# Performance work log

Hardware: AMD Instinct MI355X
Metric: run time of the kernel (lower is better)

Reference implementation:

```python
import jax, jax.numpy as jnp
import numpy as np

B, S, D, H = 2, 2048, 512, 8
DK = D // H


def setup_inputs() -> dict:
    key = jax.random.key(0)
    ks = jax.random.split(key, 7)
    scale = 1.0 / np.sqrt(D)
    return {
        "query": jax.random.normal(ks[0], (B, S, D), dtype=jnp.float32),
        "key": jax.random.normal(ks[1], (B, S, D), dtype=jnp.float32),
        "value": jax.random.normal(ks[2], (B, S, D), dtype=jnp.float32),
        "w_q": jax.random.normal(ks[3], (D, D), dtype=jnp.float32) * scale,
        "w_k": jax.random.normal(ks[4], (D, D), dtype=jnp.float32) * scale,
        "w_v": jax.random.normal(ks[5], (D, D), dtype=jnp.float32) * scale,
        "w_o": jax.random.normal(ks[6], (D, D), dtype=jnp.float32) * scale,
    }


def reference(query, key, value, w_q, w_k, w_v, w_o):
    # Linear projections (torch nn.Linear: x @ W.T), split into heads -> [b, h, s, dk]
    def proj(x, w):
        return (x @ w.T).reshape(B, -1, H, DK).transpose(0, 2, 1, 3)

    q = proj(query, w_q)
    k = proj(key, w_k)
    v = proj(value, w_v)

    # scaled dot-product attention (unfused, materializes [b,h,s,s] scores)
    scores = jnp.einsum("bhqd,bhkd->bhqk", q, k) / np.sqrt(DK)
    p_attn = jax.nn.softmax(scores, axis=-1)
    out = jnp.einsum("bhqk,bhkd->bhqd", p_attn, v)  # [b,h,s,dk]

    # merge heads and final projection
    out = out.transpose(0, 2, 1, 3).reshape(B, -1, D)
    out = out @ w_o.T
    return (out, p_attn)
```

## Files before the change

### kernel.cpp

```cpp
#include <hip/hip_runtime.h>
#include <hip/hip_bf16.h>
#include <cstdint>
#include <cstddef>

#define BB 2
#define SS 2048
#define DD 512
#define HH 8
#define DKK 64

typedef __attribute__((ext_vector_type(8))) short bf16x8;
typedef __attribute__((ext_vector_type(4))) float f32x4;

__device__ __forceinline__ unsigned short f2bf(float f) {
    union { float f; unsigned u; } v; v.f = f;
    unsigned u = v.u;
    return (unsigned short)((u + 0x7fffu + ((u >> 16) & 1u)) >> 16);
}
__device__ __forceinline__ unsigned pack2(float a, float b) {
    return (unsigned)f2bf(a) | ((unsigned)f2bf(b) << 16);
}

typedef const __attribute__((address_space(1))) unsigned int* gp_t;
typedef __attribute__((address_space(3))) unsigned int* lp_t;
__device__ __forceinline__ void gload_lds16(const void* g, void* l) {
    __builtin_amdgcn_global_load_lds((gp_t)g, (lp_t)l, 16, 0, 0);
}

#define VM_WAIT4 asm volatile("s_waitcnt vmcnt(4)" ::: "memory")
#define VM_WAIT0 asm volatile("s_waitcnt vmcnt(0)" ::: "memory")

__global__ __launch_bounds__(256) void k_cvt(
    const float* __restrict__ q, const float* __restrict__ k, const float* __restrict__ v,
    const float* __restrict__ wq, const float* __restrict__ wk, const float* __restrict__ wv,
    const float* __restrict__ wo, unsigned short* __restrict__ dst,
    unsigned short* __restrict__ dwo)
{
    const size_t NX = (size_t)BB * SS * DD;
    const size_t NW = (size_t)DD * DD;
    const int y = blockIdx.y;
    const float* src; unsigned short* d; int n;
    switch (y) {
        case 0: src = q;  d = dst;                 n = (int)NX; break;
        case 1: src = k;  d = dst + NX;            n = (int)NX; break;
        case 2: src = v;  d = dst + 2 * NX;        n = (int)NX; break;
        case 3: src = wq; d = dst + 3 * NX;        n = (int)NW; break;
        case 4: src = wk; d = dst + 3 * NX + NW;   n = (int)NW; break;
        case 5: src = wv; d = dst + 3 * NX + 2*NW; n = (int)NW; break;
        default: src = wo; d = dwo;                n = (int)NW; break;
    }
    int idx = (blockIdx.x * 256 + threadIdx.x) * 8;
    if (idx >= n) return;
    float4 a = *(const float4*)(src + idx);
    float4 b = *(const float4*)(src + idx + 4);
    *(uint4*)(d + idx) = make_uint4(pack2(a.x,a.y), pack2(a.z,a.w), pack2(b.x,b.y), pack2(b.z,b.w));
}

__device__ __forceinline__ void gemm64_core(
    const unsigned short* __restrict__ A, const unsigned short* __restrict__ W,
    unsigned short* smem, int bm, int bn, int tid, f32x4 acc[4])
{
    const int w = tid >> 6, lane = tid & 63, quad = lane >> 4, l15 = lane & 15;
    for (int k0 = 0; k0 < DD; k0 += 64) {
        #pragma unroll
        for (int r = 0; r < 2; ++r) {
            int flat = r * 256 + tid;
            int row = flat >> 3, c = flat & 7, cs = c ^ (row & 7);
            gload_lds16(A + (size_t)(bm * 64 + row) * DD + k0 + cs * 8, &smem[flat * 8]);
        }
        #pragma unroll
        for (int r = 0; r < 2; ++r) {
            int flat = r * 256 + tid;
            int row = flat >> 3, c = flat & 7, cs = c ^ (row & 7);
            gload_lds16(W + (size_t)(bn * 64 + row) * DD + k0 + cs * 8, &smem[4096 + flat * 8]);
        }
        __syncthreads();
        int mrow = w * 16 + l15;
        bf16x8 a0 = *(const bf16x8*)&smem[(mrow * 8 + (quad ^ (mrow & 7))) * 8];
        bf16x8 a1 = *(const bf16x8*)&smem[(mrow * 8 + ((quad + 4) ^ (mrow & 7))) * 8];
        #pragma unroll
        for (int nt = 0; nt < 4; ++nt) {
            int nrow = nt * 16 + l15;
            bf16x8 b0 = *(const bf16x8*)&smem[4096 + (nrow * 8 + (quad ^ (nrow & 7))) * 8];
            bf16x8 b1 = *(const bf16x8*)&smem[4096 + (nrow * 8 + ((quad + 4) ^ (nrow & 7))) * 8];
            acc[nt] = __builtin_amdgcn_mfma_f32_16x16x32_bf16(a0, b0, acc[nt], 0, 0, 0);
            acc[nt] = __builtin_amdgcn_mfma_f32_16x16x32_bf16(a1, b1, acc[nt], 0, 0, 0);
        }
        __syncthreads();
    }
}

__global__ __launch_bounds__(256) void k_gemm_qkv(
    const unsigned short* __restrict__ scratch,
    unsigned short* __restrict__ Qw, unsigned short* __restrict__ Kw,
    unsigned short* __restrict__ Vt)
{
    __shared__ unsigned short smem[8192];
    const size_t NX = (size_t)BB * SS * DD, NW = (size_t)DD * DD;
    const int z = blockIdx.z;
    const unsigned short* A = scratch + (size_t)z * NX;
    const unsigned short* W = scratch + 3 * NX + (size_t)z * NW;
    const int bm = blockIdx.x, bn = blockIdx.y;
    const int tid = threadIdx.x, w = tid >> 6, lane = tid & 63, quad = lane >> 4, l15 = lane & 15;

    f32x4 acc[4];
    #pragma unroll
    for (int i = 0; i < 4; ++i) acc[i] = (f32x4){0.f, 0.f, 0.f, 0.f};
    gemm64_core(A, W, smem, bm, bn, tid, acc);

    if (z != 2) {
        const float sc = (z == 0) ? 0.125f : 1.0f;
        unsigned short* dbf = (z == 0) ? Qw : Kw;
        #pragma unroll
        for (int nt = 0; nt < 4; ++nt) {
            int n = bn * 64 + nt * 16 + l15;
            int h = n >> 6, dk = n & 63;
            #pragma unroll
            for (int rg = 0; rg < 4; ++rg) {
                int m = bm * 64 + w * 16 + quad * 4 + rg;
                int b = m >> 11, s = m & (SS - 1);
                dbf[(((size_t)(b * HH + h) * SS + s) << 6) + dk] = f2bf(acc[nt][rg] * sc);
            }
        }
    } else {
        unsigned short* T = smem;
        #pragma unroll
        for (int nt = 0; nt < 4; ++nt)
            #pragma unroll
            for (int rg = 0; rg < 4; ++rg)
                T[(w * 16 + quad * 4 + rg) * 72 + nt * 16 + l15] = f2bf(acc[nt][rg]);
        __syncthreads();
        int n = tid >> 2, s0 = (tid & 3) * 16;
        int ng = bn * 64 + n, h = ng >> 6, dk = ng & 63;
        int mg = bm * 64 + s0, b = mg >> 11, s = mg & (SS - 1);
        unsigned vals[8];
        #pragma unroll
        for (int i = 0; i < 8; ++i)
            vals[i] = (unsigned)T[(s0 + 2*i) * 72 + n] | ((unsigned)T[(s0 + 2*i + 1) * 72 + n] << 16);
        unsigned short* dp = Vt + ((size_t)(b * HH + h) * DKK + dk) * SS + s;
        ((uint4*)dp)[0] = make_uint4(vals[0], vals[1], vals[2], vals[3]);
        ((uint4*)dp)[1] = make_uint4(vals[4], vals[5], vals[6], vals[7]);
    }
}

__global__ __launch_bounds__(256) void k_attn(
    const unsigned short* __restrict__ Qw, const unsigned short* __restrict__ Kw,
    const unsigned short* __restrict__ Vt, unsigned short* __restrict__ AO,
    float* __restrict__ Linv)
{
    __shared__ unsigned short Kl[2][4096];
    __shared__ unsigned short Vl[2][4096];
    __shared__ unsigned short Pl[2][4][16][68];

    const int id = blockIdx.x;
    const int xcd = id & 7, j = id >> 3;
    const int bh = xcd * 2 + (j >> 5), qt = j & 31;

    const int tid = threadIdx.x, w = tid >> 6, lane = tid & 63, quad = lane >> 4, l15 = lane & 15;

    const unsigned short* Qb = Qw + ((size_t)bh * SS + qt * 64 + w * 16) * DKK;
    const unsigned short* Kb = Kw + (size_t)bh * SS * DKK;
    const unsigned short* Vb = Vt + (size_t)bh * DKK * SS;

    bf16x8 qa0 = *(const bf16x8*)&Qb[l15 * DKK + quad * 8];
    bf16x8 qa1 = *(const bf16x8*)&Qb[l15 * DKK + 32 + quad * 8];

    f32x4 oacc[4];
    #pragma unroll
    for (int i = 0; i < 4; ++i) oacc[i] = (f32x4){0.f, 0.f, 0.f, 0.f};
    float lsum[4] = {0.f, 0.f, 0.f, 0.f};

    auto stage = [&](int kt, int b) {
        #pragma unroll
        for (int r = 0; r < 2; ++r) {
            int flat = r * 256 + tid;
            int row = flat >> 3, c = flat & 7, cs = c ^ (row & 7);
            gload_lds16(Kb + (size_t)(kt * 64 + row) * DKK + cs * 8, &Kl[b][flat * 8]);
        }
        #pragma unroll
        for (int r = 0; r < 2; ++r) {
            int flat = r * 256 + tid;
            int row = flat >> 3, c = flat & 7, cs = c ^ (row & 7);
            gload_lds16(Vb + (size_t)row * SS + kt * 64 + cs * 8, &Vl[b][flat * 8]);
        }
    };

    stage(0, 0);
    stage(1, 1);

    const int NT = SS / 64;
    for (int kt = 0; kt < NT; ++kt) {
        if (kt < NT - 1) { VM_WAIT4; } else { VM_WAIT0; }
        __builtin_amdgcn_s_barrier();
        __builtin_amdgcn_sched_barrier(0);
        const int b = kt & 1;

        f32x4 sa[4];
        #pragma unroll
        for (int i = 0; i < 4; ++i) sa[i] = (f32x4){0.f, 0.f, 0.f, 0.f};
        __builtin_amdgcn_s_setprio(1);
        #pragma unroll
        for (int jt = 0; jt < 4; ++jt) {
            int row = jt * 16 + l15;
            bf16x8 b0 = *(const bf16x8*)&Kl[b][(row * 8 + (quad ^ (row & 7))) * 8];
            bf16x8 b1 = *(const bf16x8*)&Kl[b][(row * 8 + ((quad + 4) ^ (row & 7))) * 8];
            sa[jt] = __builtin_amdgcn_mfma_f32_16x16x32_bf16(qa0, b0, sa[jt], 0, 0, 0);
            sa[jt] = __builtin_amdgcn_mfma_f32_16x16x32_bf16(qa1, b1, sa[jt], 0, 0, 0);
        }
        __builtin_amdgcn_s_setprio(0);

        float ev[4][4];
        #pragma unroll
        for (int jt = 0; jt < 4; ++jt)
            #pragma unroll
            for (int rg = 0; rg < 4; ++rg)
                ev[jt][rg] = __expf(sa[jt][rg]);
        #pragma unroll
        for (int rg = 0; rg < 4; ++rg) {
            float s = ev[0][rg] + ev[1][rg] + ev[2][rg] + ev[3][rg];
            s += __shfl_xor(s, 1);
            s += __shfl_xor(s, 2);
            s += __shfl_xor(s, 4);
            s += __shfl_xor(s, 8);
            lsum[rg] += s;
        }
        #pragma unroll
        for (int jt = 0; jt < 4; ++jt)
            #pragma unroll
            for (int rg = 0; rg < 4; ++rg)
                Pl[b][w][quad * 4 + rg][jt * 16 + l15] = f2bf(ev[jt][rg]);
        bf16x8 pa0 = *(const bf16x8*)&Pl[b][w][l15][quad * 8];
        bf16x8 pa1 = *(const bf16x8*)&Pl[b][w][l15][32 + quad * 8];

        __builtin_amdgcn_s_setprio(1);
        #pragma unroll
        for (int dt = 0; dt < 4; ++dt) {
            int row = dt * 16 + l15;
            bf16x8 v0 = *(const bf16x8*)&Vl[b][(row * 8 + (quad ^ (row & 7))) * 8];
            bf16x8 v1 = *(const bf16x8*)&Vl[b][(row * 8 + ((quad + 4) ^ (row & 7))) * 8];
            oacc[dt] = __builtin_amdgcn_mfma_f32_16x16x32_bf16(pa0, v0, oacc[dt], 0, 0, 0);
            oacc[dt] = __builtin_amdgcn_mfma_f32_16x16x32_bf16(pa1, v1, oacc[dt], 0, 0, 0);
        }
        __builtin_amdgcn_s_setprio(0);

        __builtin_amdgcn_s_barrier();
        if (kt + 2 < NT) stage(kt + 2, b);
    }

    float linv[4];
    #pragma unroll
    for (int rg = 0; rg < 4; ++rg) linv[rg] = 1.0f / lsum[rg];

    const int b2 = bh >> 3, h = bh & 7;
    const int srow = qt * 64 + w * 16 + quad * 4;
    #pragma unroll
    for (int dt = 0; dt < 4; ++dt)
        #pragma unroll
        for (int rg = 0; rg < 4; ++rg)
            AO[((size_t)(b2 * SS + srow + rg) << 9) + h * 64 + dt * 16 + l15] =
                f2bf(oacc[dt][rg] * linv[rg]);

    if (l15 == 0) {
        #pragma unroll
        for (int rg = 0; rg < 4; ++rg)
            Linv[(size_t)bh * SS + srow + rg] = linv[rg];
    }
}

__global__ __launch_bounds__(256) void k_pwrite(
    const unsigned short* __restrict__ Qw, const unsigned short* __restrict__ Kw,
    const float* __restrict__ Linv, float* __restrict__ P)
{
    __shared__ float Tl[4][16][68];
    const int id = blockIdx.x;
    const int xcd = id & 7, j = id >> 3;
    const int bh = xcd * 2 + (j >> 7);
    const int rem = j & 127, qt = rem >> 2, ks = rem & 3;
    const int tid = threadIdx.x, w = tid >> 6, lane = tid & 63, quad = lane >> 4, l15 = lane & 15;

    const unsigned short* Qb = Qw + ((size_t)bh * SS + qt * 64 + w * 16) * DKK;
    bf16x8 qa0 = *(const bf16x8*)&Qb[l15 * DKK + quad * 8];
    bf16x8 qa1 = *(const bf16x8*)&Qb[l15 * DKK + 32 + quad * 8];

    float linv[4];
    #pragma unroll
    for (int rg = 0; rg < 4; ++rg)
        linv[rg] = Linv[(size_t)bh * SS + qt * 64 + w * 16 + quad * 4 + rg];

    const unsigned short* Kb = Kw + (size_t)bh * SS * DKK + (size_t)ks * 512 * DKK;
    float* Pb = P + (((size_t)bh * SS + qt * 64 + w * 16) << 11) + ks * 512;

    for (int kt = 0; kt < 8; ++kt) {
        const unsigned short* Kt = Kb + (size_t)kt * 64 * DKK;
        #pragma unroll
        for (int jt = 0; jt < 4; ++jt) {
            bf16x8 b0 = *(const bf16x8*)&Kt[(jt * 16 + l15) * DKK + quad * 8];
            bf16x8 b1 = *(const bf16x8*)&Kt[(jt * 16 + l15) * DKK + 32 + quad * 8];
            f32x4 sa = (f32x4){0.f, 0.f, 0.f, 0.f};
            sa = __builtin_amdgcn_mfma_f32_16x16x32_bf16(qa0, b0, sa, 0, 0, 0);
            sa = __builtin_amdgcn_mfma_f32_16x16x32_bf16(qa1, b1, sa, 0, 0, 0);
            #pragma unroll
            for (int rg = 0; rg < 4; ++rg)
                Tl[w][quad * 4 + rg][jt * 16 + l15] = __expf(sa[rg]) * linv[rg];
        }
        #pragma unroll
        for (int c = 0; c < 4; ++c) {
            int row = c * 4 + quad;
            f32x4 val = *(const f32x4*)&Tl[w][row][l15 * 4];
            __builtin_nontemporal_store(val,
                (f32x4*)(Pb + ((size_t)row << 11) + kt * 64 + l15 * 4));
        }
    }
}

__global__ __launch_bounds__(256) void k_gemm_o(
    const unsigned short* __restrict__ A, const unsigned short* __restrict__ W,
    float* __restrict__ out)
{
    __shared__ unsigned short smem[8192];
    const int bm = blockIdx.x, bn = blockIdx.y;
    const int tid = threadIdx.x, w = tid >> 6, lane = tid & 63, quad = lane >> 4, l15 = lane & 15;
    f32x4 acc[4];
    #pragma unroll
    for (int i = 0; i < 4; ++i) acc[i] = (f32x4){0.f, 0.f, 0.f, 0.f};
    gemm64_core(A, W, smem, bm, bn, tid, acc);
    #pragma unroll
    for (int nt = 0; nt < 4; ++nt)
        #pragma unroll
        for (int rg = 0; rg < 4; ++rg)
            out[(size_t)(bm * 64 + w * 16 + quad * 4 + rg) * DD + bn * 64 + nt * 16 + l15] =
                acc[nt][rg];
}

extern "C" void kernel_launch(void* const* d_in, const int* in_sizes, int n_in,
                              void* d_out, int out_size, void* d_ws, size_t ws_size,
                              hipStream_t stream) {
    const float* q  = (const float*)d_in[0];
    const float* k  = (const float*)d_in[1];
    const float* v  = (const float*)d_in[2];
    const float* wq = (const float*)d_in[3];
    const float* wk = (const float*)d_in[4];
    const float* wv = (const float*)d_in[5];
    const float* wo = (const float*)d_in[6];

    float* out = (float*)d_out;
    float* P   = out + (size_t)BB * SS * DD;

    const size_t NX = (size_t)BB * SS * DD;
    const size_t NW = (size_t)DD * DD;

    unsigned short* scratch = (unsigned short*)P;

    unsigned short* Qw   = (unsigned short*)d_ws;
    unsigned short* Kw   = Qw + NX;
    unsigned short* Vt   = Kw + NX;
    unsigned short* AO   = Vt + NX;
    unsigned short* Wo2  = AO + NX;
    float*          Linv = (float*)(Wo2 + NW);

    k_cvt<<<dim3(1024, 7), 256, 0, stream>>>(q, k, v, wq, wk, wv, wo, scratch, Wo2);
    k_gemm_qkv<<<dim3(64, 8, 3), 256, 0, stream>>>(scratch, Qw, Kw, Vt);
    k_attn<<<dim3(512), 256, 0, stream>>>(Qw, Kw, Vt, AO, Linv);
    k_pwrite<<<dim3(2048), 256, 0, stream>>>(Qw, Kw, Linv, P);
    k_gemm_o<<<dim3(64, 8), 256, 0, stream>>>(AO, Wo2, out);
}
```

Before: 393.5 us.

## Fuse fp32-to-bf16 conversion into GEMM tile loads with register prefetch

Removes the separate conversion kernel. The QKV and output projection GEMMs now read fp32 inputs and weights directly, convert them to bf16 in registers, and write them into LDS. The next k-tile is loaded into registers while the current one is computed, giving a simple software pipeline. This drops one launch and the write and re-read of a bf16 scratch copy. In exchange, weights are re-read and re-converted by every block in fp32, so global traffic per tile doubles, and register pressure goes up.

```diff
diff --git a/kernel.cpp b/kernel.cpp
--- a/kernel.cpp
+++ b/kernel.cpp
@@ -30,51 +30,63 @@
 #define VM_WAIT4 asm volatile("s_waitcnt vmcnt(4)" ::: "memory")
 #define VM_WAIT0 asm volatile("s_waitcnt vmcnt(0)" ::: "memory")
 
-__global__ __launch_bounds__(256) void k_cvt(
-    const float* __restrict__ q, const float* __restrict__ k, const float* __restrict__ v,
-    const float* __restrict__ wq, const float* __restrict__ wk, const float* __restrict__ wv,
-    const float* __restrict__ wo, unsigned short* __restrict__ dst,
-    unsigned short* __restrict__ dwo)
-{
-    const size_t NX = (size_t)BB * SS * DD;
-    const size_t NW = (size_t)DD * DD;
-    const int y = blockIdx.y;
-    const float* src; unsigned short* d; int n;
-    switch (y) {
-        case 0: src = q;  d = dst;                 n = (int)NX; break;
-        case 1: src = k;  d = dst + NX;            n = (int)NX; break;
-        case 2: src = v;  d = dst + 2 * NX;        n = (int)NX; break;
-        case 3: src = wq; d = dst + 3 * NX;        n = (int)NW; break;
-        case 4: src = wk; d = dst + 3 * NX + NW;   n = (int)NW; break;
-        case 5: src = wv; d = dst + 3 * NX + 2*NW; n = (int)NW; break;
-        default: src = wo; d = dwo;                n = (int)NW; break;
-    }
-    int idx = (blockIdx.x * 256 + threadIdx.x) * 8;
-    if (idx >= n) return;
-    float4 a = *(const float4*)(src + idx);
-    float4 b = *(const float4*)(src + idx + 4);
-    *(uint4*)(d + idx) = make_uint4(pack2(a.x,a.y), pack2(a.z,a.w), pack2(b.x,b.y), pack2(b.z,b.w));
-}
-
-__device__ __forceinline__ void gemm64_core(
-    const unsigned short* __restrict__ A, const unsigned short* __restrict__ W,
+template <bool ABF>
+__device__ __forceinline__ void gemm64_core2(
+    const void* __restrict__ Av, const float* __restrict__ W,
     unsigned short* smem, int bm, int bn, int tid, f32x4 acc[4])
 {
     const int w = tid >> 6, lane = tid & 63, quad = lane >> 4, l15 = lane & 15;
-    for (int k0 = 0; k0 < DD; k0 += 64) {
+
+    float4 ra[2][2], rw[2][2];
+    auto loadRegs = [&](int k0) {
+        if (!ABF) {
+            const float* A = (const float*)Av;
+            #pragma unroll
+            for (int r = 0; r < 2; ++r) {
+                int flat = r * 256 + tid;
+                int row = flat >> 3, c = flat & 7, cs = c ^ (row & 7);
+                const float* p = A + (size_t)(bm * 64 + row) * DD + k0 + cs * 8;
+                ra[r][0] = *(const float4*)p;
+                ra[r][1] = *(const float4*)(p + 4);
+            }
+        }
         #pragma unroll
         for (int r = 0; r < 2; ++r) {
             int flat = r * 256 + tid;
             int row = flat >> 3, c = flat & 7, cs = c ^ (row & 7);
-            gload_lds16(A + (size_t)(bm * 64 + row) * DD + k0 + cs * 8, &smem[flat * 8]);
-        }
+            const float* p = W + (size_t)(bn * 64 + row) * DD + k0 + cs * 8;
+            rw[r][0] = *(const float4*)p;
+            rw[r][1] = *(const float4*)(p + 4);
+        }
+    };
+    auto writeLDS = [&]() {
         #pragma unroll
         for (int r = 0; r < 2; ++r) {
             int flat = r * 256 + tid;
-            int row = flat >> 3, c = flat & 7, cs = c ^ (row & 7);
-            gload_lds16(W + (size_t)(bn * 64 + row) * DD + k0 + cs * 8, &smem[4096 + flat * 8]);
-        }
+            if (!ABF)
+                *(uint4*)&smem[flat * 8] = make_uint4(
+                    pack2(ra[r][0].x, ra[r][0].y), pack2(ra[r][0].z, ra[r][0].w),
+                    pack2(ra[r][1].x, ra[r][1].y), pack2(ra[r][1].z, ra[r][1].w));
+            *(uint4*)&smem[4096 + flat * 8] = make_uint4(
+                pack2(rw[r][0].x, rw[r][0].y), pack2(rw[r][0].z, rw[r][0].w),
+                pack2(rw[r][1].x, rw[r][1].y), pack2(rw[r][1].z, rw[r][1].w));
+        }
+    };
+
+    loadRegs(0);
+    for (int k0 = 0; k0 < DD; k0 += 64) {
+        if (ABF) {
+            const unsigned short* A = (const unsigned short*)Av;
+            #pragma unroll
+            for (int r = 0; r < 2; ++r) {
+                int flat = r * 256 + tid;
+                int row = flat >> 3, c = flat & 7, cs = c ^ (row & 7);
+                gload_lds16(A + (size_t)(bm * 64 + row) * DD + k0 + cs * 8, &smem[flat * 8]);
+            }
+        }
+        writeLDS();
         __syncthreads();
+        if (k0 + 64 < DD) loadRegs(k0 + 64);
         int mrow = w * 16 + l15;
         bf16x8 a0 = *(const bf16x8*)&smem[(mrow * 8 + (quad ^ (mrow & 7))) * 8];
         bf16x8 a1 = *(const bf16x8*)&smem[(mrow * 8 + ((quad + 4) ^ (mrow & 7))) * 8];
@@ -91,22 +103,22 @@
 }
 
 __global__ __launch_bounds__(256) void k_gemm_qkv(
-    const unsigned short* __restrict__ scratch,
+    const float* __restrict__ xq, const float* __restrict__ xk, const float* __restrict__ xv,
+    const float* __restrict__ wq, const float* __restrict__ wk, const float* __restrict__ wv,
     unsigned short* __restrict__ Qw, unsigned short* __restrict__ Kw,
     unsigned short* __restrict__ Vt)
 {
     __shared__ unsigned short smem[8192];
-    const size_t NX = (size_t)BB * SS * DD, NW = (size_t)DD * DD;
     const int z = blockIdx.z;
-    const unsigned short* A = scratch + (size_t)z * NX;
-    const unsigned short* W = scratch + 3 * NX + (size_t)z * NW;
+    const float* A = (z == 0) ? xq : (z == 1) ? xk : xv;
+    const float* W = (z == 0) ? wq : (z == 1) ? wk : wv;
     const int bm = blockIdx.x, bn = blockIdx.y;
     const int tid = threadIdx.x, w = tid >> 6, lane = tid & 63, quad = lane >> 4, l15 = lane & 15;
 
     f32x4 acc[4];
     #pragma unroll
     for (int i = 0; i < 4; ++i) acc[i] = (f32x4){0.f, 0.f, 0.f, 0.f};
-    gemm64_core(A, W, smem, bm, bn, tid, acc);
+    gemm64_core2<false>(A, W, smem, bm, bn, tid, acc);
 
     if (z != 2) {
         const float sc = (z == 0) ? 0.125f : 1.0f;
@@ -314,7 +326,7 @@
 }
 
 __global__ __launch_bounds__(256) void k_gemm_o(
-    const unsigned short* __restrict__ A, const unsigned short* __restrict__ W,
+    const unsigned short* __restrict__ A, const float* __restrict__ W,
     float* __restrict__ out)
 {
     __shared__ unsigned short smem[8192];
@@ -323,7 +335,7 @@
     f32x4 acc[4];
     #pragma unroll
     for (int i = 0; i < 4; ++i) acc[i] = (f32x4){0.f, 0.f, 0.f, 0.f};
-    gemm64_core(A, W, smem, bm, bn, tid, acc);
+    gemm64_core2<true>(A, W, smem, bm, bn, tid, acc);
     #pragma unroll
     for (int nt = 0; nt < 4; ++nt)
         #pragma unroll
@@ -347,20 +359,15 @@
     float* P   = out + (size_t)BB * SS * DD;
 
     const size_t NX = (size_t)BB * SS * DD;
-    const size_t NW = (size_t)DD * DD;
-
-    unsigned short* scratch = (unsigned short*)P;
 
     unsigned short* Qw   = (unsigned short*)d_ws;
     unsigned short* Kw   = Qw + NX;
     unsigned short* Vt   = Kw + NX;
     unsigned short* AO   = Vt + NX;
-    unsigned short* Wo2  = AO + NX;
-    float*          Linv = (float*)(Wo2 + NW);
-
-    k_cvt<<<dim3(1024, 7), 256, 0, stream>>>(q, k, v, wq, wk, wv, wo, scratch, Wo2);
-    k_gemm_qkv<<<dim3(64, 8, 3), 256, 0, stream>>>(scratch, Qw, Kw, Vt);
+    float*          Linv = (float*)(AO + NX);
+
+    k_gemm_qkv<<<dim3(64, 8, 3), 256, 0, stream>>>(q, k, v, wq, wk, wv, Qw, Kw, Vt);
     k_attn<<<dim3(512), 256, 0, stream>>>(Qw, Kw, Vt, AO, Linv);
     k_pwrite<<<dim3(2048), 256, 0, stream>>>(Qw, Kw, Linv, P);
-    k_gemm_o<<<dim3(64, 8), 256, 0, stream>>>(AO, Wo2, out);
-}
+    k_gemm_o<<<dim3(64, 8), 256, 0, stream>>>(AO, wo, out);
+}
```

Result: no change. 400.0 us (+1.6%).
